# Optimization experiments

Hardware: AMD Instinct MI355X
Metric: run time of the kernel (lower is better)

Reference implementation:

```python
import jax, jax.numpy as jnp
import numpy as np

N = 100000
NNZ = 3200000
K = 3

def setup_inputs() -> dict:
    key = jax.random.key(0)
    ks = jax.random.split(key, 9)
    return {
        "x": jax.random.normal(ks[0], (N, 128), dtype=jnp.float32),
        "vals": jax.random.uniform(ks[1], (NNZ,), dtype=jnp.float32) * (1.0 / 32.0),
        "W1": jax.random.normal(ks[2], (128 * K, 256), dtype=jnp.float32) * 0.05,
        "b1": jax.random.normal(ks[3], (256,), dtype=jnp.float32) * 0.05,
        "W2": jax.random.normal(ks[4], (256 * K, 64), dtype=jnp.float32) * 0.05,
        "b2": jax.random.normal(ks[5], (64,), dtype=jnp.float32) * 0.05,
        "rows": jax.random.randint(ks[6], (NNZ,), 0, N, dtype=jnp.int32),
        "cols": jax.random.randint(ks[7], (NNZ,), 0, N, dtype=jnp.int32),
        "idx": jax.random.randint(ks[8], (50000,), 0, N, dtype=jnp.int32),
    }

def _spmm(rows, cols, vals, x):
    # sparse [N,N] @ dense [N,F] via gather + segment_sum
    return jax.ops.segment_sum(vals[:, None] * x[cols], rows, num_segments=N)

def _cheb_basis(x, rows, cols, vals, k):
    # Chebyshev recurrence: T0=x, T1=L x, T_m = 2 L T_{m-1} - T_{m-2}
    xs = [x]
    if k > 1:
        x0, x1 = x, _spmm(rows, cols, vals, x)
        xs.append(x1)
        for _ in range(2, k):
            x2 = 2.0 * _spmm(rows, cols, vals, x1) - x0
            xs.append(x2)
            x0, x1 = x1, x2
    # match torch layout: [N, F, K] -> [N, F*K] (per-feature K contiguous)
    return jnp.stack(xs, axis=2).reshape(x.shape[0], -1)

def reference(x, vals, W1, b1, W2, b2, rows, cols, idx):
    h = _cheb_basis(x, rows, cols, vals, K) @ W1 + b1
    h = jax.nn.relu(h)  # dropout omitted (eval mode)
    out = _cheb_basis(h, rows, cols, vals, K) @ W2 + b2
    return out[idx]
```

## Files before the change

kernel.cpp:

```cpp
#include <hip/hip_runtime.h>
#include <hip/hip_bf16.h>

typedef __attribute__((ext_vector_type(8))) __bf16 bf16x8;
typedef __attribute__((ext_vector_type(4))) float floatx4;
typedef unsigned short ushort_t;
typedef unsigned int uint_t;

#define N_NODES 100000
#define NNZ_E   3200000
#define N_IDX   50000
#define NB_BKT  196
#define PTILE   8192
#define PBLOCKS 391

__device__ __forceinline__ float bf2f(uint_t u16) {
  union { float f; uint_t i; } v; v.i = u16 << 16; return v.f;
}
__device__ __forceinline__ unsigned short f2bf(float f) {
  union { float f; uint_t i; } v; v.f = f;
  uint_t x = v.i;
  return (unsigned short)((x + 0x7FFFu + ((x >> 16) & 1u)) >> 16);
}


__global__ __launch_bounds__(256) void k_bhist(const int* __restrict__ rows,
                                               int* __restrict__ bcnt) {
  __shared__ int h[NB_BKT];
  for (int i = threadIdx.x; i < NB_BKT; i += 256) h[i] = 0;
  __syncthreads();
  int base = blockIdx.x * PTILE;
  for (int i = threadIdx.x; i < PTILE; i += 256) {
    int e = base + i;
    if (e < NNZ_E) atomicAdd(&h[rows[e] >> 9], 1);
  }
  __syncthreads();
  for (int i = threadIdx.x; i < NB_BKT; i += 256)
    if (h[i]) atomicAdd(&bcnt[i], h[i]);
}

__global__ void k_bscan(const int* __restrict__ bcnt, int* __restrict__ bbase,
                        int* __restrict__ bcur) {
  __shared__ int ts[256];
  int t = threadIdx.x;
  int v = (t < NB_BKT) ? bcnt[t] : 0;
  ts[t] = v;
  __syncthreads();
  for (int off = 1; off < 256; off <<= 1) {
    int x = ts[t];
    int a = (t >= off) ? ts[t - off] : 0;
    __syncthreads();
    ts[t] = x + a;
    __syncthreads();
  }
  if (t < NB_BKT) {
    int b = (t == 0) ? 0 : ts[t - 1];
    bbase[t] = b;
    bcur[t] = b;
  }
}

__global__ __launch_bounds__(256) void k_part(const int* __restrict__ rows,
                                              const int* __restrict__ cols,
                                              const float* __restrict__ vals,
                                              int* __restrict__ bcur,
                                              int2* __restrict__ tmp) {
  __shared__ int h[NB_BKT];
  for (int i = threadIdx.x; i < NB_BKT; i += 256) h[i] = 0;
  __syncthreads();
  int base = blockIdx.x * PTILE;
  for (int i = threadIdx.x; i < PTILE; i += 256) {
    int e = base + i;
    if (e < NNZ_E) atomicAdd(&h[rows[e] >> 9], 1);
  }
  __syncthreads();
  for (int i = threadIdx.x; i < NB_BKT; i += 256) {
    int c = h[i];
    h[i] = c ? atomicAdd(&bcur[i], c) : 0;
  }
  __syncthreads();
  for (int i = threadIdx.x; i < PTILE; i += 256) {
    int e = base + i;
    if (e < NNZ_E) {
      int rr = rows[e];
      int p = atomicAdd(&h[rr >> 9], 1);
      int2 o;
      o.x = cols[e] | ((rr & 511) << 17);
      o.y = __float_as_int(vals[e]);
      tmp[p] = o;
    }
  }
}

__global__ __launch_bounds__(512) void k_sort(const int* __restrict__ bbase,
                                              const int2* __restrict__ tmp,
                                              int2* __restrict__ edges,
                                              int* __restrict__ rowptr) {
  __shared__ int cnt[512];
  __shared__ int ts[512];
  int b = blockIdx.x, t = threadIdx.x;
  int s = bbase[b];
  int epos = (b == NB_BKT - 1) ? NNZ_E : bbase[b + 1];
  cnt[t] = 0;
  __syncthreads();
  for (int i = s + t; i < epos; i += 512)
    atomicAdd(&cnt[(tmp[i].x >> 17) & 511], 1);
  __syncthreads();
  ts[t] = cnt[t];
  __syncthreads();
  for (int off = 1; off < 512; off <<= 1) {
    int x = ts[t];
    int a = (t >= off) ? ts[t - off] : 0;
    __syncthreads();
    ts[t] = x + a;
    __syncthreads();
  }
  int pre = (t == 0) ? 0 : ts[t - 1];
  int grow = b * 512 + t;
  if (grow < N_NODES) rowptr[grow] = s + pre;
  cnt[t] = s + pre;
  __syncthreads();
  for (int i = s + t; i < epos; i += 512) {
    int2 p = tmp[i];
    int rl = (p.x >> 17) & 511;
    int pos = atomicAdd(&cnt[rl], 1);
    int2 o;
    o.x = p.x & 0x1FFFF;
    o.y = p.y;
    edges[pos] = o;
  }
  if (b == 0 && t == 0) rowptr[N_NODES] = NNZ_E;
}


__global__ void k_cvt(const float4* __restrict__ x, ushort4* __restrict__ xb) {
  int i = blockIdx.x * blockDim.x + threadIdx.x;
  if (i < N_NODES * 128 / 4) {
    float4 v = x[i];
    ushort4 o;
    o.x = f2bf(v.x); o.y = f2bf(v.y); o.z = f2bf(v.z); o.w = f2bf(v.w);
    xb[i] = o;
  }
}


__global__ void k_prepW1(const float* __restrict__ W, ushort_t* __restrict__ Wp) {
  int kp = blockIdx.x;
  int n  = threadIdx.x;
  int ch = kp >> 7;
  int f  = kp & 127;
  float v;
  if (ch == 0)      v = W[(f*3+0)*256+n] - W[(f*3+2)*256+n];
  else if (ch == 1) v = W[(f*3+1)*256+n];
  else              v = 2.0f * W[(f*3+2)*256+n];
  int kb = kp >> 5, kr = kp & 31;
  int lane = ((kr >> 3) << 4) | (n & 15);
  Wp[(((size_t)kb * 16 + (n >> 4)) * 64 + lane) * 8 + (kr & 7)] = f2bf(v);
}

__global__ void k_prepW2(const float* __restrict__ W, ushort_t* __restrict__ Wp) {
  int f = blockIdx.x;
  int c = threadIdx.x;
  int g = c >> 6, n = c & 63;
  float v;
  if (g == 0)      v = W[(f*3+0)*64+n] - W[(f*3+2)*64+n];
  else if (g == 1) v = W[(f*3+1)*64+n];
  else             v = 2.0f * W[(f*3+2)*64+n];
  int kb = f >> 5, kr = f & 31;
  int nb = c >> 4;
  int lane = ((kr >> 3) << 4) | (c & 15);
  Wp[(((size_t)kb * 12 + nb) * 64 + lane) * 8 + (kr & 7)] = f2bf(v);
}


__global__ __launch_bounds__(256) void k_spmm128(
    const int* __restrict__ rowptr, const int2* __restrict__ edges,
    const ushort_t* __restrict__ in, ushort_t* __restrict__ out) {
  int r = blockIdx.x * 4 + (threadIdx.x >> 6);
  int f = threadIdx.x & 63;
  int e0 = rowptr[r], e1 = rowptr[r + 1];
  float a0 = 0.f, a1 = 0.f;
  int e = e0;
  for (; e + 8 <= e1; e += 8) {
    int2 E[8];
#pragma unroll
    for (int j = 0; j < 8; ++j) E[j] = edges[e + j];
    uint_t q[8];
#pragma unroll
    for (int j = 0; j < 8; ++j)
      q[j] = *(const uint_t*)(in + (size_t)E[j].x * 128 + 2 * f);
#pragma unroll
    for (int j = 0; j < 8; ++j) {
      float v = __int_as_float(E[j].y);
      a0 = fmaf(v, bf2f(q[j] & 0xFFFFu), a0);
      a1 = fmaf(v, bf2f(q[j] >> 16), a1);
    }
  }
  for (; e + 4 <= e1; e += 4) {
    int2 E[4];
#pragma unroll
    for (int j = 0; j < 4; ++j) E[j] = edges[e + j];
#pragma unroll
    for (int j = 0; j < 4; ++j) {
      uint_t q = *(const uint_t*)(in + (size_t)E[j].x * 128 + 2 * f);
      float v = __int_as_float(E[j].y);
      a0 = fmaf(v, bf2f(q & 0xFFFFu), a0);
      a1 = fmaf(v, bf2f(q >> 16), a1);
    }
  }
  for (; e < e1; ++e) {
    int2 E = edges[e];
    uint_t q = *(const uint_t*)(in + (size_t)E.x * 128 + 2 * f);
    float v = __int_as_float(E.y);
    a0 = fmaf(v, bf2f(q & 0xFFFFu), a0);
    a1 = fmaf(v, bf2f(q >> 16), a1);
  }
  uint_t o = ((uint_t)f2bf(a1) << 16) | (uint_t)f2bf(a0);
  *(uint_t*)(out + (size_t)r * 128 + 2 * f) = o;
}


__global__ __launch_bounds__(256) void k_spmm64_add(
    const int* __restrict__ rowptr, const int2* __restrict__ edges,
    const ushort_t* __restrict__ p2, const ushort_t* __restrict__ p1,
    ushort_t* __restrict__ u) {
  int r = blockIdx.x * 4 + (threadIdx.x >> 6);
  int lane = threadIdx.x & 63;
  int half = lane >> 5, f = lane & 31;
  int e0 = rowptr[r], e1 = rowptr[r + 1];
  int ne = e1 - e0;
  int hs = (ne + 1) >> 1;
  int e = e0 + half * hs;
  int send = half ? e1 : (e0 + hs);
  float a0 = 0.f, a1 = 0.f;
  for (; e + 4 <= send; e += 4) {
    int2 E[4];
#pragma unroll
    for (int j = 0; j < 4; ++j) E[j] = edges[e + j];
#pragma unroll
    for (int j = 0; j < 4; ++j) {
      uint_t q = *(const uint_t*)(p2 + (size_t)E[j].x * 64 + 2 * f);
      float v = __int_as_float(E[j].y);
      a0 = fmaf(v, bf2f(q & 0xFFFFu), a0);
      a1 = fmaf(v, bf2f(q >> 16), a1);
    }
  }
  for (; e < send; ++e) {
    int2 E = edges[e];
    uint_t q = *(const uint_t*)(p2 + (size_t)E.x * 64 + 2 * f);
    float v = __int_as_float(E.y);
    a0 = fmaf(v, bf2f(q & 0xFFFFu), a0);
    a1 = fmaf(v, bf2f(q >> 16), a1);
  }
  a0 += __shfl_xor(a0, 32);
  a1 += __shfl_xor(a1, 32);
  if (half == 0) {
    uint_t pp = *(const uint_t*)(p1 + (size_t)r * 64 + 2 * f);
    float b0 = a0 + bf2f(pp & 0xFFFFu);
    float b1 = a1 + bf2f(pp >> 16);
    uint_t o = ((uint_t)f2bf(b1) << 16) | (uint_t)f2bf(b0);
    *(uint_t*)(u + (size_t)r * 64 + 2 * f) = o;
  }
}


__global__ __launch_bounds__(256) void k_spmm64_idx(
    const int* __restrict__ rowptr, const int2* __restrict__ edges,
    const ushort_t* __restrict__ u, const float* __restrict__ p0,
    const int* __restrict__ idx, float* __restrict__ out) {
  int o = blockIdx.x * 4 + (threadIdx.x >> 6);
  int r = idx[o];
  int lane = threadIdx.x & 63;
  int half = lane >> 5, f = lane & 31;
  int e0 = rowptr[r], e1 = rowptr[r + 1];
  int ne = e1 - e0;
  int hs = (ne + 1) >> 1;
  int e = e0 + half * hs;
  int send = half ? e1 : (e0 + hs);
  float a0 = 0.f, a1 = 0.f;
  for (; e + 4 <= send; e += 4) {
    int2 E[4];
#pragma unroll
    for (int j = 0; j < 4; ++j) E[j] = edges[e + j];
#pragma unroll
    for (int j = 0; j < 4; ++j) {
      uint_t q = *(const uint_t*)(u + (size_t)E[j].x * 64 + 2 * f);
      float v = __int_as_float(E[j].y);
      a0 = fmaf(v, bf2f(q & 0xFFFFu), a0);
      a1 = fmaf(v, bf2f(q >> 16), a1);
    }
  }
  for (; e < send; ++e) {
    int2 E = edges[e];
    uint_t q = *(const uint_t*)(u + (size_t)E.x * 64 + 2 * f);
    float v = __int_as_float(E.y);
    a0 = fmaf(v, bf2f(q & 0xFFFFu), a0);
    a1 = fmaf(v, bf2f(q >> 16), a1);
  }
  a0 += __shfl_xor(a0, 32);
  a1 += __shfl_xor(a1, 32);
  if (half == 0) {
    float2 b = *(const float2*)(p0 + (size_t)r * 64 + 2 * f);
    float2 w; w.x = b.x + a0; w.y = b.y + a1;
    *(float2*)(out + (size_t)o * 64 + 2 * f) = w;
  }
}


__global__ __launch_bounds__(256) void k_gemm1(
    const ushort_t* __restrict__ A0, const ushort_t* __restrict__ A1,
    const ushort_t* __restrict__ A2, const ushort_t* __restrict__ Bp,
    const float* __restrict__ bias, ushort_t* __restrict__ h) {
  int wid = (blockIdx.x * 256 + threadIdx.x) >> 6;
  int lane = threadIdx.x & 63;
  int mt = wid >> 1, ng = wid & 1;
  int mr = mt * 16 + (lane & 15);
  int ko = (lane >> 4) << 3;
  floatx4 acc[8] = {};
#pragma unroll
  for (int c = 0; c < 3; ++c) {
    const ushort_t* Ab = (c == 0 ? A0 : c == 1 ? A1 : A2) + (size_t)mr * 128 + ko;
#pragma unroll
    for (int kb = 0; kb < 4; ++kb) {
      bf16x8 a = *(const bf16x8*)(Ab + kb * 32);
      int kbg = c * 4 + kb;
      const ushort_t* Bb = Bp + (((size_t)(kbg * 16 + ng * 8)) * 64 + lane) * 8;
#pragma unroll
      for (int nt = 0; nt < 8; ++nt) {
        bf16x8 b = *(const bf16x8*)(Bb + (size_t)nt * 64 * 8);
        acc[nt] = __builtin_amdgcn_mfma_f32_16x16x32_bf16(a, b, acc[nt], 0, 0, 0);
      }
    }
  }
  int col0 = ng * 128 + (lane & 15);
  int r0 = mt * 16 + ((lane >> 4) << 2);
#pragma unroll
  for (int nt = 0; nt < 8; ++nt) {
    int col = col0 + nt * 16;
    float bv = bias[col];
#pragma unroll
    for (int rg = 0; rg < 4; ++rg) {
      float v = acc[nt][rg] + bv;
      v = v > 0.f ? v : 0.f;
      h[(size_t)(r0 + rg) * 256 + col] = f2bf(v);
    }
  }
}


__global__ __launch_bounds__(256) void k_gemm2(
    const ushort_t* __restrict__ A, const ushort_t* __restrict__ Bp,
    const float* __restrict__ bias, float* __restrict__ p0,
    ushort_t* __restrict__ p1, ushort_t* __restrict__ p2) {
  int wid = (blockIdx.x * 256 + threadIdx.x) >> 6;
  if (wid >= 18750) return;
  int lane = threadIdx.x & 63;
  int mt = wid / 3, ng = wid - mt * 3;
  int mr = mt * 16 + (lane & 15);
  int ko = (lane >> 4) << 3;
  floatx4 acc[4] = {};
  const ushort_t* Ab = A + (size_t)mr * 256 + ko;
#pragma unroll
  for (int kb = 0; kb < 8; ++kb) {
    bf16x8 a = *(const bf16x8*)(Ab + kb * 32);
    const ushort_t* Bb = Bp + (((size_t)(kb * 12 + ng * 4)) * 64 + lane) * 8;
#pragma unroll
    for (int nt = 0; nt < 4; ++nt) {
      bf16x8 b = *(const bf16x8*)(Bb + (size_t)nt * 64 * 8);
      acc[nt] = __builtin_amdgcn_mfma_f32_16x16x32_bf16(a, b, acc[nt], 0, 0, 0);
    }
  }
  int c16 = lane & 15;
  int r0 = mt * 16 + ((lane >> 4) << 2);
  if (ng == 0) {
#pragma unroll
    for (int nt = 0; nt < 4; ++nt) {
      float bv = bias[nt * 16 + c16];
#pragma unroll
      for (int rg = 0; rg < 4; ++rg)
        p0[(size_t)(r0 + rg) * 64 + nt * 16 + c16] = acc[nt][rg] + bv;
    }
  } else {
    ushort_t* dst = (ng == 1) ? p1 : p2;
#pragma unroll
    for (int nt = 0; nt < 4; ++nt)
#pragma unroll
      for (int rg = 0; rg < 4; ++rg)
        dst[(size_t)(r0 + rg) * 64 + nt * 16 + c16] = f2bf(acc[nt][rg]);
  }
}


extern "C" void kernel_launch(void* const* d_in, const int* in_sizes, int n_in,
                              void* d_out, int out_size, void* d_ws, size_t ws_size,
                              hipStream_t stream) {
  const float* x    = (const float*)d_in[0];
  const float* vals = (const float*)d_in[1];
  const float* W1   = (const float*)d_in[2];
  const float* b1   = (const float*)d_in[3];
  const float* W2   = (const float*)d_in[4];
  const float* b2   = (const float*)d_in[5];
  const int*   rows = (const int*)d_in[6];
  const int*   cols = (const int*)d_in[7];
  const int*   idx  = (const int*)d_in[8];
  float* out = (float*)d_out;

  char* w = (char*)d_ws;
  size_t off = 0;
  auto take = [&](size_t b) -> char* {
    char* p = w + off;
    off += (b + 255) & ~(size_t)255;
    return p;
  };
  int*      bcnt    = (int*)take((size_t)NB_BKT * 4);
  int*      bbase   = (int*)take((size_t)NB_BKT * 4);
  int*      bcur    = (int*)take((size_t)NB_BKT * 4);
  int*      rowptr  = (int*)take((size_t)(N_NODES + 1) * 4);
  int2*     tmp     = (int2*)take((size_t)NNZ_E * 8);
  int2*     edges   = (int2*)take((size_t)NNZ_E * 8);
  ushort_t* xb      = (ushort_t*)take((size_t)N_NODES * 128 * 2);
  ushort_t* T1a     = (ushort_t*)take((size_t)N_NODES * 128 * 2);
  ushort_t* U1      = (ushort_t*)take((size_t)N_NODES * 128 * 2);
  ushort_t* h       = (ushort_t*)take((size_t)N_NODES * 256 * 2);
  ushort_t* W1p     = (ushort_t*)take((size_t)384 * 256 * 2);
  ushort_t* W2p     = (ushort_t*)take((size_t)256 * 192 * 2);

  float*    p0 = (float*)xb;
  ushort_t* p1 = T1a;
  ushort_t* p2 = T1a + (size_t)N_NODES * 64;
  ushort_t* u  = U1;

  hipMemsetAsync(bcnt, 0, (size_t)NB_BKT * 4, stream);
  k_bhist<<<PBLOCKS, 256, 0, stream>>>(rows, bcnt);
  k_bscan<<<1, 256, 0, stream>>>(bcnt, bbase, bcur);
  k_part<<<PBLOCKS, 256, 0, stream>>>(rows, cols, vals, bcur, tmp);
  k_sort<<<NB_BKT, 512, 0, stream>>>(bbase, tmp, edges, rowptr);

  k_cvt<<<(N_NODES * 128 / 4 + 255) / 256, 256, 0, stream>>>((const float4*)x, (ushort4*)xb);
  k_prepW1<<<384, 256, 0, stream>>>(W1, W1p);
  k_prepW2<<<256, 192, 0, stream>>>(W2, W2p);

  k_spmm128<<<N_NODES / 4, 256, 0, stream>>>(rowptr, edges, xb, T1a);
  k_spmm128<<<N_NODES / 4, 256, 0, stream>>>(rowptr, edges, T1a, U1);
  k_gemm1<<<3125, 256, 0, stream>>>(xb, T1a, U1, W1p, b1, h);

  k_gemm2<<<4688, 256, 0, stream>>>(h, W2p, b2, p0, p1, p2);
  k_spmm64_add<<<N_NODES / 4, 256, 0, stream>>>(rowptr, edges, p2, p1, u);
  k_spmm64_idx<<<N_IDX / 4, 256, 0, stream>>>(rowptr, edges, u, p0, idx, out);
}
```

Before: 687.3 us.

## Pre-shift edge column indices to byte offsets and deepen gather unrolls; widen gemm1 tiles

Edge column indices are stored pre-shifted to byte offsets (col<<8), so the SpMM gathers compute addresses with a single OR instead of a 64-bit multiply-add. The 64-wide kernels shift right by one to get their row stride. Gather unroll depth rises (16 for the 128-feature kernel, 8 for the 64-feature kernels) to keep more loads in flight. gemm1 now has each wave compute all 256 output columns, so each A fragment is reused across 16 MFMAs, at the cost of more accumulator registers and half as many waves. The OR-based addressing relies on col*256 fitting in 32 bits and on the feature offset never overlapping the shifted index bits.

Measured after the change: 742.7 us. 1.08x slower.

```diff
diff --git a/kernel.cpp b/kernel.cpp
--- a/kernel.cpp
+++ b/kernel.cpp
@@ -124,7 +124,7 @@
     int rl = (p.x >> 17) & 511;
     int pos = atomicAdd(&cnt[rl], 1);
     int2 o;
-    o.x = p.x & 0x1FFFF;
+    o.x = (p.x & 0x1FFFF) << 8;
     o.y = p.y;
     edges[pos] = o;
   }
@@ -177,19 +177,21 @@
     const ushort_t* __restrict__ in, ushort_t* __restrict__ out) {
   int r = blockIdx.x * 4 + (threadIdx.x >> 6);
   int f = threadIdx.x & 63;
+  uint_t fo = (uint_t)f << 2;
+  const char* inb = (const char*)in;
   int e0 = rowptr[r], e1 = rowptr[r + 1];
   float a0 = 0.f, a1 = 0.f;
   int e = e0;
-  for (; e + 8 <= e1; e += 8) {
-    int2 E[8];
-#pragma unroll
-    for (int j = 0; j < 8; ++j) E[j] = edges[e + j];
-    uint_t q[8];
-#pragma unroll
-    for (int j = 0; j < 8; ++j)
-      q[j] = *(const uint_t*)(in + (size_t)E[j].x * 128 + 2 * f);
-#pragma unroll
-    for (int j = 0; j < 8; ++j) {
+  for (; e + 16 <= e1; e += 16) {
+    int2 E[16];
+#pragma unroll
+    for (int j = 0; j < 16; ++j) E[j] = edges[e + j];
+    uint_t q[16];
+#pragma unroll
+    for (int j = 0; j < 16; ++j)
+      q[j] = *(const uint_t*)(inb + (((uint_t)E[j].x) | fo));
+#pragma unroll
+    for (int j = 0; j < 16; ++j) {
       float v = __int_as_float(E[j].y);
       a0 = fmaf(v, bf2f(q[j] & 0xFFFFu), a0);
       a1 = fmaf(v, bf2f(q[j] >> 16), a1);
@@ -201,7 +203,7 @@
     for (int j = 0; j < 4; ++j) E[j] = edges[e + j];
 #pragma unroll
     for (int j = 0; j < 4; ++j) {
-      uint_t q = *(const uint_t*)(in + (size_t)E[j].x * 128 + 2 * f);
+      uint_t q = *(const uint_t*)(inb + (((uint_t)E[j].x) | fo));
       float v = __int_as_float(E[j].y);
       a0 = fmaf(v, bf2f(q & 0xFFFFu), a0);
       a1 = fmaf(v, bf2f(q >> 16), a1);
@@ -209,7 +211,7 @@
   }
   for (; e < e1; ++e) {
     int2 E = edges[e];
-    uint_t q = *(const uint_t*)(in + (size_t)E.x * 128 + 2 * f);
+    uint_t q = *(const uint_t*)(inb + (((uint_t)E.x) | fo));
     float v = __int_as_float(E.y);
     a0 = fmaf(v, bf2f(q & 0xFFFFu), a0);
     a1 = fmaf(v, bf2f(q >> 16), a1);
@@ -226,27 +228,32 @@
   int r = blockIdx.x * 4 + (threadIdx.x >> 6);
   int lane = threadIdx.x & 63;
   int half = lane >> 5, f = lane & 31;
+  uint_t fo = (uint_t)f << 2;
+  const char* pb = (const char*)p2;
   int e0 = rowptr[r], e1 = rowptr[r + 1];
   int ne = e1 - e0;
   int hs = (ne + 1) >> 1;
   int e = e0 + half * hs;
   int send = half ? e1 : (e0 + hs);
   float a0 = 0.f, a1 = 0.f;
-  for (; e + 4 <= send; e += 4) {
-    int2 E[4];
-#pragma unroll
-    for (int j = 0; j < 4; ++j) E[j] = edges[e + j];
-#pragma unroll
-    for (int j = 0; j < 4; ++j) {
-      uint_t q = *(const uint_t*)(p2 + (size_t)E[j].x * 64 + 2 * f);
+  for (; e + 8 <= send; e += 8) {
+    int2 E[8];
+#pragma unroll
+    for (int j = 0; j < 8; ++j) E[j] = edges[e + j];
+    uint_t q[8];
+#pragma unroll
+    for (int j = 0; j < 8; ++j)
+      q[j] = *(const uint_t*)(pb + ((((uint_t)E[j].x) >> 1) | fo));
+#pragma unroll
+    for (int j = 0; j < 8; ++j) {
       float v = __int_as_float(E[j].y);
-      a0 = fmaf(v, bf2f(q & 0xFFFFu), a0);
-      a1 = fmaf(v, bf2f(q >> 16), a1);
+      a0 = fmaf(v, bf2f(q[j] & 0xFFFFu), a0);
+      a1 = fmaf(v, bf2f(q[j] >> 16), a1);
     }
   }
   for (; e < send; ++e) {
     int2 E = edges[e];
-    uint_t q = *(const uint_t*)(p2 + (size_t)E.x * 64 + 2 * f);
+    uint_t q = *(const uint_t*)(pb + ((((uint_t)E.x) >> 1) | fo));
     float v = __int_as_float(E.y);
     a0 = fmaf(v, bf2f(q & 0xFFFFu), a0);
     a1 = fmaf(v, bf2f(q >> 16), a1);
@@ -271,27 +278,32 @@
   int r = idx[o];
   int lane = threadIdx.x & 63;
   int half = lane >> 5, f = lane & 31;
+  uint_t fo = (uint_t)f << 2;
+  const char* ub = (const char*)u;
   int e0 = rowptr[r], e1 = rowptr[r + 1];
   int ne = e1 - e0;
   int hs = (ne + 1) >> 1;
   int e = e0 + half * hs;
   int send = half ? e1 : (e0 + hs);
   float a0 = 0.f, a1 = 0.f;
-  for (; e + 4 <= send; e += 4) {
-    int2 E[4];
-#pragma unroll
-    for (int j = 0; j < 4; ++j) E[j] = edges[e + j];
-#pragma unroll
-    for (int j = 0; j < 4; ++j) {
-      uint_t q = *(const uint_t*)(u + (size_t)E[j].x * 64 + 2 * f);
+  for (; e + 8 <= send; e += 8) {
+    int2 E[8];
+#pragma unroll
+    for (int j = 0; j < 8; ++j) E[j] = edges[e + j];
+    uint_t q[8];
+#pragma unroll
+    for (int j = 0; j < 8; ++j)
+      q[j] = *(const uint_t*)(ub + ((((uint_t)E[j].x) >> 1) | fo));
+#pragma unroll
+    for (int j = 0; j < 8; ++j) {
       float v = __int_as_float(E[j].y);
-      a0 = fmaf(v, bf2f(q & 0xFFFFu), a0);
-      a1 = fmaf(v, bf2f(q >> 16), a1);
+      a0 = fmaf(v, bf2f(q[j] & 0xFFFFu), a0);
+      a1 = fmaf(v, bf2f(q[j] >> 16), a1);
     }
   }
   for (; e < send; ++e) {
     int2 E = edges[e];
-    uint_t q = *(const uint_t*)(u + (size_t)E.x * 64 + 2 * f);
+    uint_t q = *(const uint_t*)(ub + ((((uint_t)E.x) >> 1) | fo));
     float v = __int_as_float(E.y);
     a0 = fmaf(v, bf2f(q & 0xFFFFu), a0);
     a1 = fmaf(v, bf2f(q >> 16), a1);
@@ -311,11 +323,11 @@
     const ushort_t* __restrict__ A2, const ushort_t* __restrict__ Bp,
     const float* __restrict__ bias, ushort_t* __restrict__ h) {
   int wid = (blockIdx.x * 256 + threadIdx.x) >> 6;
+  if (wid >= 6250) return;
   int lane = threadIdx.x & 63;
-  int mt = wid >> 1, ng = wid & 1;
-  int mr = mt * 16 + (lane & 15);
+  int mr = wid * 16 + (lane & 15);
   int ko = (lane >> 4) << 3;
-  floatx4 acc[8] = {};
+  floatx4 acc[16] = {};
 #pragma unroll
   for (int c = 0; c < 3; ++c) {
     const ushort_t* Ab = (c == 0 ? A0 : c == 1 ? A1 : A2) + (size_t)mr * 128 + ko;
@@ -323,19 +335,19 @@
     for (int kb = 0; kb < 4; ++kb) {
       bf16x8 a = *(const bf16x8*)(Ab + kb * 32);
       int kbg = c * 4 + kb;
-      const ushort_t* Bb = Bp + (((size_t)(kbg * 16 + ng * 8)) * 64 + lane) * 8;
-#pragma unroll
-      for (int nt = 0; nt < 8; ++nt) {
+      const ushort_t* Bb = Bp + (((size_t)kbg * 16 * 64) + lane) * 8;
+#pragma unroll
+      for (int nt = 0; nt < 16; ++nt) {
         bf16x8 b = *(const bf16x8*)(Bb + (size_t)nt * 64 * 8);
         acc[nt] = __builtin_amdgcn_mfma_f32_16x16x32_bf16(a, b, acc[nt], 0, 0, 0);
       }
     }
   }
-  int col0 = ng * 128 + (lane & 15);
-  int r0 = mt * 16 + ((lane >> 4) << 2);
-#pragma unroll
-  for (int nt = 0; nt < 8; ++nt) {
-    int col = col0 + nt * 16;
+  int c16 = lane & 15;
+  int r0 = wid * 16 + ((lane >> 4) << 2);
+#pragma unroll
+  for (int nt = 0; nt < 16; ++nt) {
+    int col = nt * 16 + c16;
     float bv = bias[col];
 #pragma unroll
     for (int rg = 0; rg < 4; ++rg) {
@@ -441,7 +453,7 @@
 
   k_spmm128<<<N_NODES / 4, 256, 0, stream>>>(rowptr, edges, xb, T1a);
   k_spmm128<<<N_NODES / 4, 256, 0, stream>>>(rowptr, edges, T1a, U1);
-  k_gemm1<<<3125, 256, 0, stream>>>(xb, T1a, U1, W1p, b1, h);
+  k_gemm1<<<1563, 256, 0, stream>>>(xb, T1a, U1, W1p, b1, h);
 
   k_gemm2<<<4688, 256, 0, stream>>>(h, W2p, b2, p0, p1, p2);
   k_spmm64_add<<<N_NODES / 4, 256, 0, stream>>>(rowptr, edges, p2, p1, u);
```
